# Kernel optimization log

Measured on AMD Instinct MI355X. Metric: run time of the kernel, lower is better.

Reference implementation:

```python
import jax, jax.numpy as jnp
import numpy as np

N_NODES = 100000
N_EDGES = 1600000
IN_C = 64
HID = 64


def _glorot(key, shape):
    fan_in, fan_out = shape[1], shape[0]
    lim = (6.0 / (fan_in + fan_out)) ** 0.5
    return jax.random.uniform(key, shape, jnp.float32, -lim, lim)


def setup_inputs() -> dict:
    key = jax.random.key(0)
    ks = jax.random.split(key, 8)
    x = jax.random.normal(ks[0], (N_NODES, IN_C), jnp.float32)
    edge_index = jax.random.randint(ks[1], (2, N_EDGES), 0, N_NODES, jnp.int32)
    return {
        "x": x,
        "edge_index": edge_index,
        # conv1 (SAGEConv in->hid): lin_l (bias), lin_r (no bias)
        "W1l": _glorot(ks[2], (HID, IN_C)),
        "b1l": jnp.zeros((HID,), jnp.float32),
        "W1r": _glorot(ks[3], (HID, IN_C)),
        # conv2 (SAGEConv hid->hid)
        "W2l": _glorot(ks[4], (HID, HID)),
        "b2l": jnp.zeros((HID,), jnp.float32),
        "W2r": _glorot(ks[5], (HID, HID)),
        # edge scorer: Linear(2*hid, 1)
        "Wlin": _glorot(ks[6], (1, 2 * HID)),
        "blin": jnp.zeros((1,), jnp.float32),
    }


def _sage_conv(x, src, dst, Wl, bl, Wr, n_nodes):
    # mean aggregation of source features onto destination nodes
    agg = jax.ops.segment_sum(x[src], dst, num_segments=n_nodes)  # [N, F]
    cnt = jax.ops.segment_sum(jnp.ones((src.shape[0],), x.dtype), dst,
                              num_segments=n_nodes)  # [N]
    mean = agg / jnp.maximum(cnt, 1.0)[:, None]  # isolated nodes -> 0
    return mean @ Wl.T + bl + x @ Wr.T


def reference(x, edge_index, W1l, b1l, W1r, W2l, b2l, W2r, Wlin, blin):
    src, dst = edge_index[0], edge_index[1]
    n = x.shape[0]
    h = jax.nn.relu(_sage_conv(x, src, dst, W1l, b1l, W1r, n))
    h = jax.nn.relu(_sage_conv(h, src, dst, W2l, b2l, W2r, n))
    he = jnp.concatenate([h[src], h[dst]], axis=1)  # [E, 2*HID]
    return (he @ Wlin.T + blin).squeeze(-1)  # [E]
```

## Files before the change

kernel.cpp:

```cpp
#include <hip/hip_runtime.h>
#include <hip/hip_bf16.h>

#define N_NODES 100000
#define N_EDGES 1600000
#define NBUCK 196
#define BCAP 12288
#define CHUNK 4096
#define PART_BLOCKS 391


typedef __hip_bfloat16 bf16;
typedef short short8 __attribute__((ext_vector_type(8)));
typedef float f32x4 __attribute__((ext_vector_type(4)));
typedef unsigned int uint;

__device__ __forceinline__ short f2bs(float f) {
    bf16 h = __float2bfloat16(f);
    short s; __builtin_memcpy(&s, &h, 2); return s;
}
__device__ __forceinline__ float lo_bf(uint w) {
    uint v = w << 16; float f; __builtin_memcpy(&f, &v, 4); return f;
}
__device__ __forceinline__ float hi_bf(uint w) {
    uint v = w & 0xFFFF0000u; float f; __builtin_memcpy(&f, &v, 4); return f;
}
__device__ __forceinline__ uint pack2(float a, float b) {
    return (uint)(unsigned short)f2bs(a) | ((uint)(unsigned short)f2bs(b) << 16);
}
__device__ __forceinline__ short8 load8bf(const bf16* __restrict__ p, long idx) {
    return *(const short8*)((const short*)p + idx);
}

__global__ __launch_bounds__(256) void convert_kernel(
    const float* __restrict__ in, bf16* __restrict__ out, int* __restrict__ gcur,
    const float* __restrict__ W1l, const float* __restrict__ W1r,
    const float* __restrict__ W2l, const float* __restrict__ W2r,
    bf16* __restrict__ wb)
{
    if (blockIdx.x < 6250) {
        int i = blockIdx.x * 256 + threadIdx.x;
        float4 v = ((const float4*)in)[i];
        uint2 o;
        o.x = pack2(v.x, v.y);
        o.y = pack2(v.z, v.w);
        ((uint2*)out)[i] = o;
        if (blockIdx.x == 0) gcur[threadIdx.x] = threadIdx.x * BCAP;
    } else {
        for (int k = threadIdx.x; k < 16384; k += 256) {
            float v;
            if (k < 4096)       v = W1l[k];
            else if (k < 8192)  v = W1r[k - 4096];
            else if (k < 12288) v = W2l[k - 8192];
            else                v = W2r[k - 12288];
            wb[k] = __float2bfloat16(v);
        }
    }
}


__global__ __launch_bounds__(256) void partition_kernel(
    const int* __restrict__ src, const int* __restrict__ dst,
    int* __restrict__ gcur, int* __restrict__ pk)
{
    __shared__ int h[256], scn[256], cur[256], gb[256];
    __shared__ int pl[CHUNK];
    __shared__ unsigned char bb[CHUNK];
    int t = threadIdx.x;
    h[t] = 0;
    __syncthreads();
    int e0 = blockIdx.x * CHUNK;
    for (int i = t; i < CHUNK; i += 256) {
        int e = e0 + i;
        if (e < N_EDGES) atomicAdd(&h[dst[e] >> 9], 1);
    }
    __syncthreads();
    scn[t] = h[t];
    __syncthreads();
#pragma unroll
    for (int off = 1; off < 256; off <<= 1) {
        int add = (t >= off) ? scn[t - off] : 0;
        __syncthreads();
        scn[t] += add;
        __syncthreads();
    }
    cur[t] = scn[t] - h[t];
    __syncthreads();
    int cnt_local = scn[255];
    for (int i = t; i < CHUNK; i += 256) {
        int e = e0 + i;
        if (e < N_EDGES) {
            int d = dst[e];
            int b = d >> 9;
            int p = atomicAdd(&cur[b], 1);
            pl[p] = src[e] | ((d & 511) << 17);
            bb[p] = (unsigned char)b;
        }
    }
    __syncthreads();
    if (h[t] > 0) gb[t] = atomicAdd(&gcur[t], h[t]);
    __syncthreads();
    for (int i = t; i < cnt_local; i += 256) {
        int b = bb[i];
        int pos = gb[b] + (i - (scn[b] - h[b]));
        if (pos < (b + 1) * BCAP) pk[pos] = pl[i];
    }
}

__global__ __launch_bounds__(512) void csr_build(
    const int* __restrict__ gcur, const int* __restrict__ pk,
    int* __restrict__ csr, int2* __restrict__ node_range)
{
    __shared__ int deg[512], scn[512], cur[512];
    __shared__ int csr_l[BCAP];
    int t = threadIdx.x;
    int b = blockIdx.x;
    int base = b * BCAP;
    int cnt = gcur[b] - base;
    if (cnt > BCAP) cnt = BCAP;
    deg[t] = 0;
    __syncthreads();
    for (int i = t; i < cnt; i += 512)
        atomicAdd(&deg[pk[base + i] >> 17], 1);
    __syncthreads();
    scn[t] = deg[t];
    __syncthreads();
#pragma unroll
    for (int off = 1; off < 512; off <<= 1) {
        int add = (t >= off) ? scn[t - off] : 0;
        __syncthreads();
        scn[t] += add;
        __syncthreads();
    }
    int excl = scn[t] - deg[t];
    cur[t] = excl;
    int n = (b << 9) + t;
    if (n < N_NODES) node_range[n] = make_int2(base + excl, base + excl + deg[t]);
    __syncthreads();
    for (int i = t; i < cnt; i += 512) {
        int v = pk[base + i];
        int p = atomicAdd(&cur[v >> 17], 1);
        csr_l[p] = v & 0x1FFFF;
    }
    __syncthreads();
    for (int i = t; i < cnt; i += 512)
        csr[base + i] = csr_l[i];
}

__global__ __launch_bounds__(256) void aggregate_mean(
    const bf16* __restrict__ feat, const int2* __restrict__ node_range,
    const int* __restrict__ csr, bf16* __restrict__ mean)
{
    int wave = threadIdx.x >> 6, lane = threadIdx.x & 63;
    int g = lane >> 3, ci = lane & 7;
    int n = (blockIdx.x * 4 + wave) * 8 + g;
    int2 rg = node_range[n];
    int beg = rg.x, end = rg.y;
    const uint* fw = (const uint*)feat;
    float a0 = 0.f, a1 = 0.f, a2 = 0.f, a3 = 0.f;
    float a4 = 0.f, a5 = 0.f, a6 = 0.f, a7 = 0.f;
    int i = beg;
    for (; i + 3 < end; i += 4) {
        int s0 = csr[i], s1 = csr[i + 1], s2 = csr[i + 2], s3 = csr[i + 3];
        uint4 w0 = *(const uint4*)(fw + (long)s0 * 32 + ci * 4);
        uint4 w1 = *(const uint4*)(fw + (long)s1 * 32 + ci * 4);
        uint4 w2 = *(const uint4*)(fw + (long)s2 * 32 + ci * 4);
        uint4 w3 = *(const uint4*)(fw + (long)s3 * 32 + ci * 4);
        a0 += lo_bf(w0.x) + lo_bf(w1.x) + lo_bf(w2.x) + lo_bf(w3.x);
        a1 += hi_bf(w0.x) + hi_bf(w1.x) + hi_bf(w2.x) + hi_bf(w3.x);
        a2 += lo_bf(w0.y) + lo_bf(w1.y) + lo_bf(w2.y) + lo_bf(w3.y);
        a3 += hi_bf(w0.y) + hi_bf(w1.y) + hi_bf(w2.y) + hi_bf(w3.y);
        a4 += lo_bf(w0.z) + lo_bf(w1.z) + lo_bf(w2.z) + lo_bf(w3.z);
        a5 += hi_bf(w0.z) + hi_bf(w1.z) + hi_bf(w2.z) + hi_bf(w3.z);
        a6 += lo_bf(w0.w) + lo_bf(w1.w) + lo_bf(w2.w) + lo_bf(w3.w);
        a7 += hi_bf(w0.w) + hi_bf(w1.w) + hi_bf(w2.w) + hi_bf(w3.w);
    }
    for (; i < end; i++) {
        int s = csr[i];
        uint4 w = *(const uint4*)(fw + (long)s * 32 + ci * 4);
        a0 += lo_bf(w.x); a1 += hi_bf(w.x);
        a2 += lo_bf(w.y); a3 += hi_bf(w.y);
        a4 += lo_bf(w.z); a5 += hi_bf(w.z);
        a6 += lo_bf(w.w); a7 += hi_bf(w.w);
    }
    int d = end - beg;
    float inv = d > 0 ? 1.0f / (float)d : 0.0f;
    uint4 q;
    q.x = pack2(a0 * inv, a1 * inv);
    q.y = pack2(a2 * inv, a3 * inv);
    q.z = pack2(a4 * inv, a5 * inv);
    q.w = pack2(a6 * inv, a7 * inv);
    *(uint4*)((uint*)mean + (long)n * 32 + ci * 4) = q;
}

__device__ __forceinline__ void load_afrags(
    short8* a, const bf16* __restrict__ mean,
    const bf16* __restrict__ self, int na, int quad)
{
#pragma unroll
    for (int c = 0; c < 2; c++)
        a[c] = load8bf(mean, (long)na * 64 + c * 32 + quad * 8);
#pragma unroll
    for (int c = 0; c < 2; c++)
        a[2 + c] = load8bf(self, (long)na * 64 + c * 32 + quad * 8);
}

__device__ __forceinline__ short8 load_bfrag(
    const bf16* __restrict__ wlb, int f, int c, int quad)
{
    if (c < 2) return load8bf(wlb, (long)f * 64 + c * 32 + quad * 8);
    return load8bf(wlb, 4096 + (long)f * 64 + (c - 2) * 32 + quad * 8);
}

__global__ __launch_bounds__(256) void node_layer1_mfma(
    const bf16* __restrict__ xb, const bf16* __restrict__ mean,
    const bf16* __restrict__ wlb, const float* __restrict__ bl,
    bf16* __restrict__ h_out)
{
    int tid = threadIdx.x;
    int wave = tid >> 6, lane = tid & 63;
    int quad = lane >> 4, n16 = lane & 15;
    int nb = (blockIdx.x * 4 + wave) * 16;

    int node_a = nb + n16;
    int na = node_a < N_NODES ? node_a : N_NODES - 1;
    short8 a[4];
    load_afrags(a, mean, xb, na, quad);

#pragma unroll
    for (int t = 0; t < 4; t++) {
        int f = 16 * t + n16;
        f32x4 acc = {0.f, 0.f, 0.f, 0.f};
#pragma unroll
        for (int c = 0; c < 4; c++) {
            short8 b = load_bfrag(wlb, f, c, quad);
            acc = __builtin_amdgcn_mfma_f32_16x16x32_bf16(a[c], b, acc, 0, 0, 0);
        }
        float bias = bl[f];
#pragma unroll
        for (int r = 0; r < 4; r++) {
            int node = nb + quad * 4 + r;
            if (node < N_NODES)
                h_out[(long)node * 64 + f] = __float2bfloat16(fmaxf(acc[r] + bias, 0.0f));
        }
    }
}

__global__ __launch_bounds__(256) void node_layer2_mfma(
    const bf16* __restrict__ h1, const bf16* __restrict__ mean,
    const bf16* __restrict__ wlb, const float* __restrict__ bl,
    const float* __restrict__ Wlin,
    float* __restrict__ s_src, float* __restrict__ s_dst)
{
    int tid = threadIdx.x;
    int wave = tid >> 6, lane = tid & 63;
    int quad = lane >> 4, n16 = lane & 15;
    int nb = (blockIdx.x * 4 + wave) * 16;

    int node_a = nb + n16;
    int na = node_a < N_NODES ? node_a : N_NODES - 1;
    short8 a[4];
    load_afrags(a, mean, h1, na, quad);

    float sa[4] = {0.f, 0.f, 0.f, 0.f};
    float sb[4] = {0.f, 0.f, 0.f, 0.f};
#pragma unroll
    for (int t = 0; t < 4; t++) {
        int f = 16 * t + n16;
        f32x4 acc = {0.f, 0.f, 0.f, 0.f};
#pragma unroll
        for (int c = 0; c < 4; c++) {
            short8 b = load_bfrag(wlb, f, c, quad);
            acc = __builtin_amdgcn_mfma_f32_16x16x32_bf16(a[c], b, acc, 0, 0, 0);
        }
        float bias = bl[f];
        float wa = Wlin[f];
        float wb = Wlin[64 + f];
#pragma unroll
        for (int r = 0; r < 4; r++) {
            float h = fmaxf(acc[r] + bias, 0.0f);
            sa[r] += h * wa;
            sb[r] += h * wb;
        }
    }
#pragma unroll
    for (int m = 1; m < 16; m <<= 1) {
#pragma unroll
        for (int r = 0; r < 4; r++) {
            sa[r] += __shfl_xor(sa[r], m);
            sb[r] += __shfl_xor(sb[r], m);
        }
    }
    if (n16 == 0) {
#pragma unroll
        for (int r = 0; r < 4; r++) {
            int node = nb + quad * 4 + r;
            if (node < N_NODES) { s_src[node] = sa[r]; s_dst[node] = sb[r]; }
        }
    }
}

__global__ __launch_bounds__(256) void edge_out_kernel(
    const int* __restrict__ src, const int* __restrict__ dst,
    const float* __restrict__ s_src, const float* __restrict__ s_dst,
    const float* __restrict__ blin, float* __restrict__ out)
{
    int i = blockIdx.x * 256 + threadIdx.x;
    if (i >= N_EDGES / 4) return;
    int4 s4 = ((const int4*)src)[i];
    int4 d4 = ((const int4*)dst)[i];
    float b = blin[0];
    float4 o;
    o.x = s_src[s4.x] + s_dst[d4.x] + b;
    o.y = s_src[s4.y] + s_dst[d4.y] + b;
    o.z = s_src[s4.z] + s_dst[d4.z] + b;
    o.w = s_src[s4.w] + s_dst[d4.w] + b;
    ((float4*)out)[i] = o;
}

extern "C" void kernel_launch(void* const* d_in, const int* in_sizes, int n_in,
                              void* d_out, int out_size, void* d_ws, size_t ws_size,
                              hipStream_t stream) {
    const float* x    = (const float*)d_in[0];
    const int*   ei   = (const int*)d_in[1];
    const float* W1l  = (const float*)d_in[2];
    const float* b1l  = (const float*)d_in[3];
    const float* W1r  = (const float*)d_in[4];
    const float* W2l  = (const float*)d_in[5];
    const float* b2l  = (const float*)d_in[6];
    const float* W2r  = (const float*)d_in[7];
    const float* Wlin = (const float*)d_in[8];
    const float* blin = (const float*)d_in[9];
    float* out = (float*)d_out;

    const int* src = ei;
    const int* dst = ei + N_EDGES;

    char* w = (char*)d_ws;
    bf16*  xb    = (bf16*)w;  w += (size_t)N_NODES * 64 * 2;
    bf16*  mean  = (bf16*)w;  w += (size_t)N_NODES * 64 * 2;
    bf16*  h1    = (bf16*)w;  w += (size_t)N_NODES * 64 * 2;
    float* ssrc  = (float*)w; w += (size_t)N_NODES * 4;
    float* sdst  = (float*)w; w += (size_t)N_NODES * 4;
    int2*  nrng  = (int2*)w;  w += (size_t)N_NODES * 8;
    int*   gcur  = (int*)w;   w += 256 * 4;
    bf16*  wb    = (bf16*)w;  w += 16384 * 2;
    int*   pk    = (int*)w;   w += (size_t)NBUCK * BCAP * 4;
    int*   csr   = (int*)w;   w += (size_t)NBUCK * BCAP * 4;

    const int conv_blocks = 6251;
    const int agg_blocks  = N_NODES / 32;
    const int node_blocks = (N_NODES + 63) / 64;
    const int eo_blocks   = (N_EDGES / 4 + 255) / 256;

    convert_kernel<<<conv_blocks, 256, 0, stream>>>(x, xb, gcur, W1l, W1r, W2l, W2r, wb);
    partition_kernel<<<PART_BLOCKS, 256, 0, stream>>>(src, dst, gcur, pk);
    csr_build<<<NBUCK, 512, 0, stream>>>(gcur, pk, csr, nrng);

    aggregate_mean<<<agg_blocks, 256, 0, stream>>>(xb, nrng, csr, mean);
    node_layer1_mfma<<<node_blocks, 256, 0, stream>>>(xb, mean, wb, b1l, h1);

    aggregate_mean<<<agg_blocks, 256, 0, stream>>>(h1, nrng, csr, mean);
    node_layer2_mfma<<<node_blocks, 256, 0, stream>>>(h1, mean, wb + 8192, b2l, Wlin, ssrc, sdst);

    edge_out_kernel<<<eo_blocks, 256, 0, stream>>>(src, dst, ssrc, sdst, blin, out);
}
```

Measured before the change: 257.7 us.

## Fuse mean aggregation into MFMA node layers via LDS and use wave-shuffle scans

Measured after the change: 238.2 us. 1.08x faster.

```diff
diff --git a/kernel.cpp b/kernel.cpp
--- a/kernel.cpp
+++ b/kernel.cpp
@@ -7,6 +7,7 @@
 #define BCAP 12288
 #define CHUNK 4096
 #define PART_BLOCKS 391
+#define MSTRIDE 36
 
 
 typedef __hip_bfloat16 bf16;
@@ -74,15 +75,22 @@
         if (e < N_EDGES) atomicAdd(&h[dst[e] >> 9], 1);
     }
     __syncthreads();
-    scn[t] = h[t];
-    __syncthreads();
-#pragma unroll
-    for (int off = 1; off < 256; off <<= 1) {
-        int add = (t >= off) ? scn[t - off] : 0;
-        __syncthreads();
-        scn[t] += add;
-        __syncthreads();
-    }
+    if (t < 64) {
+        int v0 = h[t * 4], v1 = h[t * 4 + 1], v2 = h[t * 4 + 2], v3 = h[t * 4 + 3];
+        int i0 = v0, i1 = i0 + v1, i2 = i1 + v2, i3 = i2 + v3;
+        int run = i3;
+#pragma unroll
+        for (int off = 1; off < 64; off <<= 1) {
+            int u = __shfl_up(run, off);
+            if (t >= off) run += u;
+        }
+        int excl = run - i3;
+        scn[t * 4]     = excl + i0;
+        scn[t * 4 + 1] = excl + i1;
+        scn[t * 4 + 2] = excl + i2;
+        scn[t * 4 + 3] = excl + i3;
+    }
+    __syncthreads();
     cur[t] = scn[t] - h[t];
     __syncthreads();
     int cnt_local = scn[255];
@@ -122,15 +130,21 @@
     for (int i = t; i < cnt; i += 512)
         atomicAdd(&deg[pk[base + i] >> 17], 1);
     __syncthreads();
-    scn[t] = deg[t];
-    __syncthreads();
-#pragma unroll
-    for (int off = 1; off < 512; off <<= 1) {
-        int add = (t >= off) ? scn[t - off] : 0;
-        __syncthreads();
-        scn[t] += add;
-        __syncthreads();
-    }
+    if (t < 64) {
+        int e[8], inc[8], s = 0;
+#pragma unroll
+        for (int k = 0; k < 8; k++) { e[k] = deg[t * 8 + k]; s += e[k]; inc[k] = s; }
+        int run = s;
+#pragma unroll
+        for (int off = 1; off < 64; off <<= 1) {
+            int u = __shfl_up(run, off);
+            if (t >= off) run += u;
+        }
+        int excl = run - s;
+#pragma unroll
+        for (int k = 0; k < 8; k++) scn[t * 8 + k] = excl + inc[k];
+    }
+    __syncthreads();
     int excl = scn[t] - deg[t];
     cur[t] = excl;
     int n = (b << 9) + t;
@@ -146,14 +160,16 @@
         csr[base + i] = csr_l[i];
 }
 
-__global__ __launch_bounds__(256) void aggregate_mean(
+
+__device__ __forceinline__ void gather_mean_lds(
     const bf16* __restrict__ feat, const int2* __restrict__ node_range,
-    const int* __restrict__ csr, bf16* __restrict__ mean)
+    const int* __restrict__ csr, int nb0, uint* __restrict__ mean_l)
 {
     int wave = threadIdx.x >> 6, lane = threadIdx.x & 63;
     int g = lane >> 3, ci = lane & 7;
-    int n = (blockIdx.x * 4 + wave) * 8 + g;
-    int2 rg = node_range[n];
+    int nl = wave * 8 + g;
+    int n = nb0 + nl;
+    int2 rg = (n < N_NODES) ? node_range[n] : make_int2(0, 0);
     int beg = rg.x, end = rg.y;
     const uint* fw = (const uint*)feat;
     float a0 = 0.f, a1 = 0.f, a2 = 0.f, a3 = 0.f;
@@ -189,19 +205,7 @@
     q.y = pack2(a2 * inv, a3 * inv);
     q.z = pack2(a4 * inv, a5 * inv);
     q.w = pack2(a6 * inv, a7 * inv);
-    *(uint4*)((uint*)mean + (long)n * 32 + ci * 4) = q;
-}
-
-__device__ __forceinline__ void load_afrags(
-    short8* a, const bf16* __restrict__ mean,
-    const bf16* __restrict__ self, int na, int quad)
-{
-#pragma unroll
-    for (int c = 0; c < 2; c++)
-        a[c] = load8bf(mean, (long)na * 64 + c * 32 + quad * 8);
-#pragma unroll
-    for (int c = 0; c < 2; c++)
-        a[2 + c] = load8bf(self, (long)na * 64 + c * 32 + quad * 8);
+    *(uint4*)(mean_l + nl * MSTRIDE + ci * 4) = q;
 }
 
 __device__ __forceinline__ short8 load_bfrag(
@@ -211,20 +215,31 @@
     return load8bf(wlb, 4096 + (long)f * 64 + (c - 2) * 32 + quad * 8);
 }
 
-__global__ __launch_bounds__(256) void node_layer1_mfma(
-    const bf16* __restrict__ xb, const bf16* __restrict__ mean,
-    const bf16* __restrict__ wlb, const float* __restrict__ bl,
-    bf16* __restrict__ h_out)
-{
+__global__ __launch_bounds__(512) void layer1_fused(
+    const bf16* __restrict__ xb, const int2* __restrict__ nrng,
+    const int* __restrict__ csr, const bf16* __restrict__ wlb,
+    const float* __restrict__ bl, bf16* __restrict__ h_out)
+{
+    __shared__ uint mean_l[64 * MSTRIDE];
+    int nb0 = blockIdx.x * 64;
+    gather_mean_lds(xb, nrng, csr, nb0, mean_l);
+    __syncthreads();
     int tid = threadIdx.x;
     int wave = tid >> 6, lane = tid & 63;
+    if (wave >= 4) return;
     int quad = lane >> 4, n16 = lane & 15;
-    int nb = (blockIdx.x * 4 + wave) * 16;
+    int nb = nb0 + wave * 16;
+    int ln = wave * 16 + n16;
 
     int node_a = nb + n16;
     int na = node_a < N_NODES ? node_a : N_NODES - 1;
     short8 a[4];
-    load_afrags(a, mean, xb, na, quad);
+#pragma unroll
+    for (int c = 0; c < 2; c++)
+        a[c] = *(const short8*)(mean_l + ln * MSTRIDE + c * 16 + quad * 4);
+#pragma unroll
+    for (int c = 0; c < 2; c++)
+        a[2 + c] = load8bf(xb, (long)na * 64 + c * 32 + quad * 8);
 
 #pragma unroll
     for (int t = 0; t < 4; t++) {
@@ -245,21 +260,32 @@
     }
 }
 
-__global__ __launch_bounds__(256) void node_layer2_mfma(
-    const bf16* __restrict__ h1, const bf16* __restrict__ mean,
-    const bf16* __restrict__ wlb, const float* __restrict__ bl,
-    const float* __restrict__ Wlin,
+__global__ __launch_bounds__(512) void layer2_fused(
+    const bf16* __restrict__ h1, const int2* __restrict__ nrng,
+    const int* __restrict__ csr, const bf16* __restrict__ wlb,
+    const float* __restrict__ bl, const float* __restrict__ Wlin,
     float* __restrict__ s_src, float* __restrict__ s_dst)
 {
+    __shared__ uint mean_l[64 * MSTRIDE];
+    int nb0 = blockIdx.x * 64;
+    gather_mean_lds(h1, nrng, csr, nb0, mean_l);
+    __syncthreads();
     int tid = threadIdx.x;
     int wave = tid >> 6, lane = tid & 63;
+    if (wave >= 4) return;
     int quad = lane >> 4, n16 = lane & 15;
-    int nb = (blockIdx.x * 4 + wave) * 16;
+    int nb = nb0 + wave * 16;
+    int ln = wave * 16 + n16;
 
     int node_a = nb + n16;
     int na = node_a < N_NODES ? node_a : N_NODES - 1;
     short8 a[4];
-    load_afrags(a, mean, h1, na, quad);
+#pragma unroll
+    for (int c = 0; c < 2; c++)
+        a[c] = *(const short8*)(mean_l + ln * MSTRIDE + c * 16 + quad * 4);
+#pragma unroll
+    for (int c = 0; c < 2; c++)
+        a[2 + c] = load8bf(h1, (long)na * 64 + c * 32 + quad * 8);
 
     float sa[4] = {0.f, 0.f, 0.f, 0.f};
     float sb[4] = {0.f, 0.f, 0.f, 0.f};
@@ -337,7 +363,6 @@
 
     char* w = (char*)d_ws;
     bf16*  xb    = (bf16*)w;  w += (size_t)N_NODES * 64 * 2;
-    bf16*  mean  = (bf16*)w;  w += (size_t)N_NODES * 64 * 2;
     bf16*  h1    = (bf16*)w;  w += (size_t)N_NODES * 64 * 2;
     float* ssrc  = (float*)w; w += (size_t)N_NODES * 4;
     float* sdst  = (float*)w; w += (size_t)N_NODES * 4;
@@ -347,20 +372,16 @@
     int*   pk    = (int*)w;   w += (size_t)NBUCK * BCAP * 4;
     int*   csr   = (int*)w;   w += (size_t)NBUCK * BCAP * 4;
 
-    const int conv_blocks = 6251;
-    const int agg_blocks  = N_NODES / 32;
-    const int node_blocks = (N_NODES + 63) / 64;
-    const int eo_blocks   = (N_EDGES / 4 + 255) / 256;
+    const int conv_blocks  = 6251;
+    const int fused_blocks = (N_NODES + 63) / 64;
+    const int eo_blocks    = (N_EDGES / 4 + 255) / 256;
 
     convert_kernel<<<conv_blocks, 256, 0, stream>>>(x, xb, gcur, W1l, W1r, W2l, W2r, wb);
     partition_kernel<<<PART_BLOCKS, 256, 0, stream>>>(src, dst, gcur, pk);
     csr_build<<<NBUCK, 512, 0, stream>>>(gcur, pk, csr, nrng);
 
-    aggregate_mean<<<agg_blocks, 256, 0, stream>>>(xb, nrng, csr, mean);
-    node_layer1_mfma<<<node_blocks, 256, 0, stream>>>(xb, mean, wb, b1l, h1);
-
-    aggregate_mean<<<agg_blocks, 256, 0, stream>>>(h1, nrng, csr, mean);
-    node_layer2_mfma<<<node_blocks, 256, 0, stream>>>(h1, mean, wb + 8192, b2l, Wlin, ssrc, sdst);
+    layer1_fused<<<fused_blocks, 512, 0, stream>>>(xb, nrng, csr, wb, b1l, h1);
+    layer2_fused<<<fused_blocks, 512, 0, stream>>>(h1, nrng, csr, wb + 8192, b2l, Wlin, ssrc, sdst);
 
     edge_out_kernel<<<eo_blocks, 256, 0, stream>>>(src, dst, ssrc, sdst, blin, out);
 }
```
